# Optimization experiments

Hardware: AMD Instinct MI355X
Metric: run time of the kernel (lower is better)

Reference implementation:

```python
import jax, jax.numpy as jnp
import numpy as np

N = 100000
E = 800000
IN_CH = 128
HID = 32
HEADS = 8
OUT_CH = 40
NEG_SLOPE = 0.2


def setup_inputs() -> dict:
    key = jax.random.key(0)
    ks = jax.random.split(key, 10)
    x = jax.random.normal(ks[0], (N, IN_CH), dtype=jnp.float32)
    edge_index = jax.random.randint(ks[1], (2, E), 0, N, dtype=jnp.int64)
    # GATConv layer 1: in -> heads*hid, concat=True
    s1 = 1.0 / np.sqrt(IN_CH)
    W1 = jax.random.uniform(ks[2], (IN_CH, HEADS * HID), jnp.float32, -s1, s1)
    att_src1 = jax.random.uniform(ks[3], (1, HEADS, HID), jnp.float32, -s1, s1)
    att_dst1 = jax.random.uniform(ks[4], (1, HEADS, HID), jnp.float32, -s1, s1)
    b1 = jnp.zeros((HEADS * HID,), jnp.float32)
    # GATConv layer 2: heads*hid -> out, heads=1, concat=True
    s2 = 1.0 / np.sqrt(HEADS * HID)
    W2 = jax.random.uniform(ks[5], (HEADS * HID, OUT_CH), jnp.float32, -s2, s2)
    att_src2 = jax.random.uniform(ks[6], (1, 1, OUT_CH), jnp.float32, -s2, s2)
    att_dst2 = jax.random.uniform(ks[7], (1, 1, OUT_CH), jnp.float32, -s2, s2)
    b2 = jnp.zeros((OUT_CH,), jnp.float32)
    return {"x": x, "edge_index": edge_index,
            "W1": W1, "att_src1": att_src1, "att_dst1": att_dst1, "b1": b1,
            "W2": W2, "att_src2": att_src2, "att_dst2": att_dst2, "b2": b2}


def _gat_layer(x, src, dst, W, att_src, att_dst, bias, heads, out_ch):
    n = x.shape[0]
    xp = (x @ W).reshape(n, heads, out_ch)               # [N,H,C]
    a_src = jnp.sum(xp * att_src, axis=-1)               # [N,H]
    a_dst = jnp.sum(xp * att_dst, axis=-1)               # [N,H]
    logits = a_src[src] + a_dst[dst]                      # [Etot,H]
    logits = jnp.where(logits > 0, logits, NEG_SLOPE * logits)  # leaky_relu
    # segment softmax over destination node
    m = jax.ops.segment_max(logits, dst, num_segments=n)  # [N,H]
    p = jnp.exp(logits - m[dst])
    z = jax.ops.segment_sum(p, dst, num_segments=n)
    alpha = p / (z[dst] + 1e-16)                           # [Etot,H]
    out = jax.ops.segment_sum(xp[src] * alpha[:, :, None], dst, num_segments=n)
    return out.reshape(n, heads * out_ch) + bias


def reference(x, edge_index, W1, att_src1, att_dst1, b1, W2, att_src2, att_dst2, b2):
    n = x.shape[0]
    # add self loops (PyG GATConv default add_self_loops=True)
    loop = jnp.arange(n, dtype=edge_index.dtype)
    src = jnp.concatenate([edge_index[0], loop])
    dst = jnp.concatenate([edge_index[1], loop])
    # dropout p=0.2 is identity in eval mode
    h = _gat_layer(x, src, dst, W1, att_src1, att_dst1, b1, HEADS, HID)
    h = jax.nn.relu(h)
    out = _gat_layer(h, src, dst, W2, att_src2, att_dst2, b2, 1, OUT_CH)
    return jax.nn.log_softmax(out, axis=1)
```

## Files before the change

### kernel.cpp

```cpp
#include <hip/hip_runtime.h>
#include <math.h>

#define NN 100000
#define NE 800000
#define C1 256
#define OC 40
#define XPAD 64
#define NEG 0.2f
#define FCHUNK 4096
#define G1BLK 1563

typedef _Float16 h4 __attribute__((ext_vector_type(4)));
typedef _Float16 h8 __attribute__((ext_vector_type(8)));
typedef float f4v __attribute__((ext_vector_type(4)));
typedef float f2v __attribute__((ext_vector_type(2)));

static __device__ __forceinline__ float leaky(float v){ return v > 0.f ? v : NEG*v; }

static __device__ __forceinline__ h8 mk8(float4 a, float4 b){
  h8 r = {(_Float16)a.x,(_Float16)a.y,(_Float16)a.z,(_Float16)a.w,
          (_Float16)b.x,(_Float16)b.y,(_Float16)b.z,(_Float16)b.w};
  return r;
}

static __device__ __forceinline__ void gload_lds16(const float* g, float* l){
  __builtin_amdgcn_global_load_lds((const __attribute__((address_space(1))) void*)g,
                                   (__attribute__((address_space(3))) void*)l, 16, 0, 0);
}


__global__ __launch_bounds__(256) void k_wt(const float* __restrict__ W1, const float* __restrict__ W2,
                                            const float* __restrict__ aS1, const float* __restrict__ aD1,
                                            const float* __restrict__ aS2, const float* __restrict__ aD2,
                                            _Float16* __restrict__ W1t, _Float16* __restrict__ W2t,
                                            int* __restrict__ deg){
  int b = blockIdx.x;
  if (b < 128){
    int k = b, nb = threadIdx.x;
    W1t[(size_t)nb*128 + k] = (_Float16)W1[k*256 + nb];
  } else if (b < 176){
    int nb = b - 128;
    int e = threadIdx.x;
    int l = e >> 2, j = e & 3;
    int k = (l>>5)*128 + ((l>>4)&1)*64 + j*16 + (l&15);
    float v = (nb < OC) ? W2[(size_t)k*OC + nb] : 0.f;
    W2t[(size_t)nb*256 + e] = (_Float16)v;
  } else if (b < 178){
    int b2 = b - 176;
    int h  = threadIdx.x >> 5;
    int kb = (threadIdx.x & 31) * 4;
    const float* att = b2 ? aD1 : aS1;
    #pragma unroll
    for (int kk = 0; kk < 4; ++kk){
      int k = kb + kk;
      float s = 0.f;
      for (int c = 0; c < 32; ++c) s += W1[k*256 + h*32 + c] * att[h*32 + c];
      W1t[(size_t)(256 + b2*8 + h)*128 + k] = (_Float16)s;
    }
  } else if (b < 194){
    int j = b - 178;
    int e = threadIdx.x;
    int l = e >> 2, jj = e & 3;
    int k = (l>>5)*128 + ((l>>4)&1)*64 + jj*16 + (l&15);
    float v = 0.f;
    if (j == 0){ for (int c = 0; c < OC; ++c) v += W2[(size_t)k*OC + c] * aS2[c]; }
    else if (j == 1){ for (int c = 0; c < OC; ++c) v += W2[(size_t)k*OC + c] * aD2[c]; }
    W2t[(size_t)(48 + j)*256 + e] = (_Float16)v;
  } else {
    int i = (b - 194)*256 + threadIdx.x;
    if (i < NN) deg[i] = 1;
  }
}

__global__ __launch_bounds__(256) void k_gemm1(const float* __restrict__ x,
    const _Float16* __restrict__ W1t, unsigned* __restrict__ xp1w,
    float* __restrict__ asrc, float* __restrict__ adst,
    const int* __restrict__ ei, int* __restrict__ deg)
{
  __shared__ float xs[64*128];
  if (blockIdx.x >= G1BLK){
    int i = (blockIdx.x - G1BLK)*256 + threadIdx.x;
    if (i < NE) atomicAdd(&deg[ei[NE + i]], 1);
    return;
  }
  const int tid  = threadIdx.x;
  const int lane = tid & 63;
  const int w    = tid >> 6;
  const int wr = w >> 1, wc = w & 1;
  const int n = lane & 15, quad = lane >> 4;
  const int r0 = blockIdx.x * 64;

  if (r0 + 64 <= NN){
    #pragma unroll
    for (int it = 0; it < 8; ++it){
      int idx = it*256 + tid;
      int row = idx >> 5, c16 = idx & 31;
      const float* src = x + (size_t)(r0 + row)*128 + ((c16 ^ (row & 7)) << 2);
      gload_lds16(src, xs + ((size_t)(it*256 + w*64) << 2));
    }
  } else {
    #pragma unroll
    for (int it = 0; it < 8; ++it){
      int idx = it*256 + tid;
      int row = idx >> 5, c16 = idx & 31;
      int gr = r0 + row; gr = gr < NN ? gr : NN-1;
      ((float4*)xs)[idx] = *(const float4*)(x + (size_t)gr*128 + ((c16 ^ (row & 7)) << 2));
    }
  }

  h8 b0[9];
  #pragma unroll
  for (int ct = 0; ct < 8; ++ct)
    b0[ct] = *(const h8*)(W1t + (size_t)(wc*128 + ct*16 + n)*128 + quad*8);
  if (wc == 0) b0[8] = *(const h8*)(W1t + (size_t)(256 + n)*128 + quad*8);

  __syncthreads();

  f4v acc[2][8];
  #pragma unroll
  for (int rt = 0; rt < 2; ++rt)
    #pragma unroll
    for (int ct = 0; ct < 8; ++ct) acc[rt][ct] = (f4v){0.f,0.f,0.f,0.f};
  f4v accE0 = {0.f,0.f,0.f,0.f}, accE1 = {0.f,0.f,0.f,0.f};

  const int rowA = wr*32 + n;
  const int rowB = rowA + 16;
  const int s = n & 7;

  #pragma unroll
  for (int ks = 0; ks < 4; ++ks){
    const int base16 = ks*8 + quad*2;
    float4 fa0 = ((const float4*)xs)[rowA*32 + ((base16    ) ^ s)];
    float4 fa1 = ((const float4*)xs)[rowA*32 + ((base16 + 1) ^ s)];
    float4 fb0 = ((const float4*)xs)[rowB*32 + ((base16    ) ^ s)];
    float4 fb1 = ((const float4*)xs)[rowB*32 + ((base16 + 1) ^ s)];
    h8 a0 = mk8(fa0, fa1);
    h8 a1 = mk8(fb0, fb1);
    #pragma unroll
    for (int ct = 0; ct < 8; ++ct){
      h8 b = (ks == 0) ? b0[ct]
           : *(const h8*)(W1t + (size_t)(wc*128 + ct*16 + n)*128 + ks*32 + quad*8);
      acc[0][ct] = __builtin_amdgcn_mfma_f32_16x16x32_f16(a0, b, acc[0][ct], 0, 0, 0);
      acc[1][ct] = __builtin_amdgcn_mfma_f32_16x16x32_f16(a1, b, acc[1][ct], 0, 0, 0);
    }
    if (wc == 0){
      h8 b = (ks == 0) ? b0[8]
           : *(const h8*)(W1t + (size_t)(256 + n)*128 + ks*32 + quad*8);
      accE0 = __builtin_amdgcn_mfma_f32_16x16x32_f16(a0, b, accE0, 0, 0, 0);
      accE1 = __builtin_amdgcn_mfma_f32_16x16x32_f16(a1, b, accE1, 0, 0, 0);
    }
  }

  #pragma unroll
  for (int rt = 0; rt < 2; ++rt){
    #pragma unroll
    for (int reg = 0; reg < 4; ++reg){
      const int row = r0 + wr*32 + rt*16 + quad*4 + reg;
      if (row < NN){
        float v[8];
        #pragma unroll
        for (int ct = 0; ct < 8; ++ct) v[ct] = acc[rt][ct][reg];
        unsigned dwA = (unsigned)__builtin_amdgcn_cvt_pk_fp8_f32(v[0], v[1], 0, false);
        dwA = (unsigned)__builtin_amdgcn_cvt_pk_fp8_f32(v[2], v[3], (int)dwA, true);
        unsigned dwB = (unsigned)__builtin_amdgcn_cvt_pk_fp8_f32(v[4], v[5], 0, false);
        dwB = (unsigned)__builtin_amdgcn_cvt_pk_fp8_f32(v[6], v[7], (int)dwB, true);
        unsigned* xr = xp1w + (size_t)row*64 + wc*32 + n;
        xr[0]  = dwA;
        xr[16] = dwB;
        if (wc == 0){
          float vE = (rt == 0) ? accE0[reg] : accE1[reg];
          if (n < 8) asrc[row*8 + n] = vE;
          else       adst[row*8 + (n - 8)] = vE;
        }
      }
    }
  }
}

__global__ __launch_bounds__(256) void k_scan1(const int* __restrict__ deg, int* part, int* bsum){
  __shared__ int lds[256];
  const int t = threadIdx.x;
  const int base = blockIdx.x*1024;
  int v[4]; int s = 0;
  #pragma unroll
  for (int i = 0; i < 4; ++i){ int idx = base + t*4 + i; v[i] = (idx < NN) ? deg[idx] : 0; s += v[i]; }
  lds[t] = s; __syncthreads();
  for (int off = 1; off < 256; off <<= 1){
    int xx = (t >= off) ? lds[t-off] : 0;
    __syncthreads();
    lds[t] += xx;
    __syncthreads();
  }
  int excl = lds[t] - s;
  #pragma unroll
  for (int i = 0; i < 4; ++i){ int idx = base + t*4 + i; if (idx < NN) part[idx] = excl; excl += v[i]; }
  if (t == 255) bsum[blockIdx.x] = lds[255];
}
__global__ void k_scan2(const int* __restrict__ bsum, int* boff){
  const int l = threadIdx.x;
  int a = (l      < 98) ? bsum[l]      : 0;
  int b = (64 + l < 98) ? bsum[64 + l] : 0;
  int sa = a, sb = b;
  #pragma unroll
  for (int off = 1; off < 64; off <<= 1){
    int ta = __shfl_up(sa, off, 64);
    int tb = __shfl_up(sb, off, 64);
    if (l >= off){ sa += ta; sb += tb; }
  }
  const int totalA = __shfl(sa, 63, 64);
  if (l      < 98) boff[l]      = sa - a;
  if (64 + l < 98) boff[64 + l] = totalA + sb - b;
}
__global__ __launch_bounds__(256) void k_scan3(const int* __restrict__ part, const int* __restrict__ boff,
                                               int* rowptr, int* cursor){
  int i = blockIdx.x*256 + threadIdx.x;
  if (i < NN){ int v = part[i] + boff[i >> 10]; rowptr[i] = v; cursor[i] = v; }
  if (i == 0) rowptr[NN] = NN + NE;
}
__global__ __launch_bounds__(256) void k_fill(const int* __restrict__ ei, int* cursor, int* __restrict__ esrc){
  const int xcd = blockIdx.x & 7;
  const int base = (blockIdx.x >> 3) * FCHUNK;
  const int lo = xcd * (NN/8), hi = lo + (NN/8);
  const int end = (base + FCHUNK < NE + NN) ? (base + FCHUNK) : (NE + NN);
  for (int i = base + threadIdx.x; i < end; i += 256){
    int s, d;
    if (i < NE){ s = ei[i]; d = ei[NE + i]; } else { s = d = i - NE; }
    if (d >= lo && d < hi){
      int slot = atomicAdd(&cursor[d], 1);
      esrc[slot] = s;
    }
  }
}

template<int B>
static __device__ __forceinline__ void agg1_batch(
    const int j0, const int je, const int lane,
    const int* __restrict__ esrc, const float* __restrict__ asrc,
    const float adA, const float adB,
    const unsigned* __restrict__ xp1w,
    f2v& accLo, f2v& accHi, float& z0, float& z1)
{
  const int cnt = je - j0;
  const int slot = lane & 15;
  const int hA = (lane >> 4) << 1;
  int idx = j0 + slot; idx = idx < je ? idx : je - 1;
  const int sv = esrc[idx];
  float pv0 = 0.f, pv1 = 0.f;
  if (slot < cnt){
    f2v av = *(const f2v*)(asrc + (size_t)sv*8 + hA);
    pv0 = __expf(leaky(av.x + adA));
    pv1 = __expf(leaky(av.y + adB));
  }
  z0 += pv0; z1 += pv1;
  unsigned u[B];
  #pragma unroll
  for (int e = 0; e < B; ++e){
    int s = __builtin_amdgcn_readlane(sv, e);
    u[e] = xp1w[(size_t)s*64 + lane];
  }
  __builtin_amdgcn_sched_barrier(0);
  const int pb = lane & 48;
  #pragma unroll
  for (int e = 0; e < B; ++e){
    const float pA = __shfl(pv0, pb | e, 64);
    const float pB = __shfl(pv1, pb | e, 64);
    f2v lo = __builtin_amdgcn_cvt_pk_f32_fp8((int)u[e], false);
    f2v hi = __builtin_amdgcn_cvt_pk_f32_fp8((int)u[e], true);
    accLo += (f2v){pA, pA} * lo;
    accHi += (f2v){pB, pB} * hi;
  }
}

__global__ __launch_bounds__(256) void k_agg1(const unsigned* __restrict__ xp1w,
    const float* __restrict__ asrc, const float* __restrict__ adst,
    const float* __restrict__ b1, const int* __restrict__ rowptr,
    const int* __restrict__ esrc, _Float16* __restrict__ h1)
{
  const int lane = threadIdx.x & 63;
  int n = __builtin_amdgcn_readfirstlane(blockIdx.x*4 + (threadIdx.x >> 6));
  const int hA = (lane >> 4) << 1;
  const f2v ad = *(const f2v*)(adst + (size_t)n*8 + hA);
  const int jb = rowptr[n], je = rowptr[n+1];
  const int cbase = (lane>>5)*128 + ((lane>>4)&1)*64 + (lane&15);
  const float bp0 = b1[cbase], bp1 = b1[cbase+16], bp2 = b1[cbase+32], bp3 = b1[cbase+48];
  f2v accLo = {0.f,0.f}, accHi = {0.f,0.f};
  float z0 = 0.f, z1 = 0.f;

  int j0 = jb;
  while (j0 < je){
    if (je - j0 > 8){
      agg1_batch<16>(j0, je, lane, esrc, asrc, ad.x, ad.y, xp1w, accLo, accHi, z0, z1);
      j0 += 16;
    } else {
      agg1_batch<8>(j0, je, lane, esrc, asrc, ad.x, ad.y, xp1w, accLo, accHi, z0, z1);
      j0 += 8;
    }
  }
  #pragma unroll
  for (int off = 1; off <= 8; off <<= 1){
    z0 += __shfl_xor(z0, off, 64);
    z1 += __shfl_xor(z1, off, 64);
  }
  const float invA = 1.f/(z0 + 1e-16f), invB = 1.f/(z1 + 1e-16f);
  h4 o = {(_Float16)fmaxf(accLo.x*invA + bp0, 0.f),
          (_Float16)fmaxf(accLo.y*invA + bp1, 0.f),
          (_Float16)fmaxf(accHi.x*invB + bp2, 0.f),
          (_Float16)fmaxf(accHi.y*invB + bp3, 0.f)};
  ((h4*)h1)[(size_t)n*64 + lane] = o;
}

__global__ __launch_bounds__(256) void k_gemm2(const _Float16* __restrict__ h1,
    const _Float16* __restrict__ W2t, _Float16* __restrict__ xp2,
    float* __restrict__ asrc2, float* __restrict__ adst2)
{
  const int tid  = threadIdx.x;
  const int lane = tid & 63;
  const int w    = tid >> 6;
  const int n = lane & 15, quad = lane >> 4;
  const int r0 = blockIdx.x * 64 + w*16;

  f4v acc[4];
  #pragma unroll
  for (int ct = 0; ct < 4; ++ct) acc[ct] = (f4v){0.f,0.f,0.f,0.f};

  int rr = r0 + n; rr = rr < NN ? rr : NN-1;

  #pragma unroll
  for (int ks = 0; ks < 8; ++ks){
    h8 a = *(const h8*)(h1 + (size_t)rr*256 + ks*32 + quad*8);
    #pragma unroll
    for (int ct = 0; ct < 4; ++ct){
      h8 b = *(const h8*)(W2t + (size_t)(ct*16 + n)*256 + ks*32 + quad*8);
      acc[ct] = __builtin_amdgcn_mfma_f32_16x16x32_f16(a, b, acc[ct], 0, 0, 0);
    }
  }

  #pragma unroll
  for (int reg = 0; reg < 4; ++reg){
    const int row = r0 + quad*4 + reg;
    if (row < NN){
      float v0 = acc[0][reg], v1 = acc[1][reg], v2 = acc[2][reg], v3 = acc[3][reg];
      _Float16* xr = xp2 + (size_t)row*XPAD + n;
      xr[0]  = (_Float16)v0;
      xr[16] = (_Float16)v1;
      if (n < 8) xr[32] = (_Float16)v2;
      if (n == 0) asrc2[row] = v3;
      if (n == 1) adst2[row] = v3;
    }
  }
}

__global__ __launch_bounds__(256) void k_agg2(const _Float16* __restrict__ xp2,
    const float* __restrict__ asrc2, const float* __restrict__ adst2,
    const float* __restrict__ b2, const int* __restrict__ rowptr,
    const int* __restrict__ esrc, float* __restrict__ out)
{
  const int lane = threadIdx.x & 63;
  const int g = lane >> 4;
  const int t = lane & 15;
  int n = __builtin_amdgcn_readfirstlane(blockIdx.x*4 + (threadIdx.x >> 6));
  const float ad = adst2[n];
  const int jb = rowptr[n], je = rowptr[n+1];
  f4v acc = {0.f,0.f,0.f,0.f};
  float zacc = 0.f;

  for (int j0 = jb; j0 < je; j0 += 16){
    const int cnt = je - j0;
    int idx = j0 + t; idx = idx < je ? idx : je - 1;
    const int sv = esrc[idx];
    const float pv = (t < cnt) ? __expf(leaky(asrc2[sv] + ad)) : 0.f;
    zacc += pv;
    h4 u[4];
    #pragma unroll
    for (int e4 = 0; e4 < 4; ++e4){
      int svg = __shfl(sv, e4*4 + g, 64);
      u[e4] = *(const h4*)(xp2 + (size_t)svg*XPAD + t*4);
    }
    __builtin_amdgcn_sched_barrier(0);
    #pragma unroll
    for (int e4 = 0; e4 < 4; ++e4){
      const float p = __shfl(pv, e4*4 + g, 64);
      acc.x += p*(float)u[e4].x;
      acc.y += p*(float)u[e4].y;
      acc.z += p*(float)u[e4].z;
      acc.w += p*(float)u[e4].w;
    }
  }
  #pragma unroll
  for (int off = 1; off <= 8; off <<= 1) zacc += __shfl_xor(zacc, off, 64);
  #pragma unroll
  for (int off = 16; off <= 32; off <<= 1){
    acc.x += __shfl_xor(acc.x, off, 64);
    acc.y += __shfl_xor(acc.y, off, 64);
    acc.z += __shfl_xor(acc.z, off, 64);
    acc.w += __shfl_xor(acc.w, off, 64);
  }
  const float inv = 1.f/(zacc + 1e-16f);
  const bool act = t < 10;
  float4 bv = act ? *(const float4*)(b2 + 4*t) : make_float4(0.f,0.f,0.f,0.f);
  float v0 = acc.x*inv + bv.x, v1 = acc.y*inv + bv.y;
  float v2 = acc.z*inv + bv.z, v3 = acc.w*inv + bv.w;
  float m = act ? fmaxf(fmaxf(v0,v1), fmaxf(v2,v3)) : -INFINITY;
  #pragma unroll
  for (int off = 1; off <= 8; off <<= 1) m = fmaxf(m, __shfl_xor(m, off, 64));
  float es = act ? (__expf(v0-m)+__expf(v1-m)+__expf(v2-m)+__expf(v3-m)) : 0.f;
  #pragma unroll
  for (int off = 1; off <= 8; off <<= 1) es += __shfl_xor(es, off, 64);
  if (lane < 10){
    float lse = m + __logf(es);
    float4 o = make_float4(v0-lse, v1-lse, v2-lse, v3-lse);
    *(float4*)(out + (size_t)n*OC + 4*t) = o;
  }
}

extern "C" void kernel_launch(void* const* d_in, const int* in_sizes, int n_in,
                              void* d_out, int out_size, void* d_ws, size_t ws_size,
                              hipStream_t stream)
{
  const float* x   = (const float*)d_in[0];
  const int*   ei  = (const int*)  d_in[1];
  const float* W1  = (const float*)d_in[2];
  const float* aS1 = (const float*)d_in[3];
  const float* aD1 = (const float*)d_in[4];
  const float* b1  = (const float*)d_in[5];
  const float* W2  = (const float*)d_in[6];
  const float* aS2 = (const float*)d_in[7];
  const float* aD2 = (const float*)d_in[8];
  const float* b2  = (const float*)d_in[9];
  float* out = (float*)d_out;

  char* wsp = (char*)d_ws;
  size_t off = 0;
  auto alloc = [&](size_t bytes){ void* p = wsp + off; off += (bytes + 255) & ~(size_t)255; return p; };
  unsigned* xp1w = (unsigned*)alloc((size_t)NN*C1);
  _Float16* h1  = (_Float16*)alloc((size_t)NN*C1*2);
  float* as1  = (float*)alloc((size_t)NN*8*4);
  float* ad1  = (float*)alloc((size_t)NN*8*4);
  float* as2  = (float*)alloc((size_t)NN*4);
  float* ad2  = (float*)alloc((size_t)NN*4);
  int* deg    = (int*)alloc((size_t)NN*4);
  int* part   = (int*)alloc((size_t)NN*4);
  int* rowptr = (int*)alloc((size_t)(NN+1)*4);
  int* cursor = (int*)alloc((size_t)NN*4);
  int* bsum   = (int*)alloc(98*4);
  int* boff   = (int*)alloc(98*4);
  int* esrc   = (int*)alloc((size_t)(NN+NE)*4);
  _Float16* W1t = (_Float16*)alloc((size_t)272*128*2);
  _Float16* W2t = (_Float16*)alloc((size_t)64*256*2);
  _Float16* xp2 = (_Float16*)alloc((size_t)NN*XPAD*2);
  (void)ws_size; (void)in_sizes; (void)n_in; (void)out_size;

  const int fill_chunks = (NE + NN + FCHUNK - 1) / FCHUNK;
  const int deg_blocks  = (NE + 255) / 256;

  k_wt    <<<194 + (NN + 255)/256, 256, 0, stream>>>(W1, W2, aS1, aD1, aS2, aD2, W1t, W2t, deg);
  k_gemm1 <<<G1BLK + deg_blocks,   256, 0, stream>>>(x, W1t, xp1w, as1, ad1, ei, deg);
  k_scan1 <<<98,   256, 0, stream>>>(deg, part, bsum);
  k_scan2 <<<1,    64,  0, stream>>>(bsum, boff);
  k_scan3 <<<391,  256, 0, stream>>>(part, boff, rowptr, cursor);
  k_fill  <<<fill_chunks*8, 256, 0, stream>>>(ei, cursor, esrc);
  k_agg1  <<<25000,256, 0, stream>>>(xp1w, as1, ad1, b1, rowptr, esrc, h1);
  k_gemm2 <<<1563, 256, 0, stream>>>(h1, W2t, xp2, as2, ad2);
  k_agg2  <<<25000,256, 0, stream>>>(xp2, as2, ad2, b2, rowptr, esrc, out);
}
```

Measured before the change: 337.5 us.

## Restructure layer-1 GEMM to per-wave 16-row tiles loading x directly to registers

Replaces the shared-memory staged 64x128 x tile (loaded via global_load_lds with swizzle) with each wave loading its own 16 rows of x straight into registers. Each wave now computes all 256 output columns plus the attention column (17 MFMA tiles), so there is no LDS usage and no __syncthreads. This removes LDS traffic and the barrier and may raise occupancy, at the cost of each wave reading all of W1t (more global/L2 traffic for weights) and holding 17 accumulators in registers.

```diff
diff --git a/kernel.cpp b/kernel.cpp
--- a/kernel.cpp
+++ b/kernel.cpp
@@ -21,11 +21,6 @@
   h8 r = {(_Float16)a.x,(_Float16)a.y,(_Float16)a.z,(_Float16)a.w,
           (_Float16)b.x,(_Float16)b.y,(_Float16)b.z,(_Float16)b.w};
   return r;
-}
-
-static __device__ __forceinline__ void gload_lds16(const float* g, float* l){
-  __builtin_amdgcn_global_load_lds((const __attribute__((address_space(1))) void*)g,
-                                   (__attribute__((address_space(3))) void*)l, 16, 0, 0);
 }
 
 
@@ -77,7 +72,6 @@
     float* __restrict__ asrc, float* __restrict__ adst,
     const int* __restrict__ ei, int* __restrict__ deg)
 {
-  __shared__ float xs[64*128];
   if (blockIdx.x >= G1BLK){
     int i = (blockIdx.x - G1BLK)*256 + threadIdx.x;
     if (i < NE) atomicAdd(&deg[ei[NE + i]], 1);
@@ -86,93 +80,57 @@
   const int tid  = threadIdx.x;
   const int lane = tid & 63;
   const int w    = tid >> 6;
-  const int wr = w >> 1, wc = w & 1;
   const int n = lane & 15, quad = lane >> 4;
-  const int r0 = blockIdx.x * 64;
-
-  if (r0 + 64 <= NN){
+  const int r0 = blockIdx.x * 64 + w*16;
+
+  int ra = r0 + n; ra = ra < NN ? ra : NN-1;
+  const float* xr = x + (size_t)ra*128 + quad*8;
+
+  float4 fa[4][2];
+  #pragma unroll
+  for (int ks = 0; ks < 4; ++ks){
+    fa[ks][0] = *(const float4*)(xr + ks*32);
+    fa[ks][1] = *(const float4*)(xr + ks*32 + 4);
+  }
+
+  f4v acc[17];
+  #pragma unroll
+  for (int ct = 0; ct < 17; ++ct) acc[ct] = (f4v){0.f,0.f,0.f,0.f};
+
+  #pragma unroll
+  for (int ks = 0; ks < 4; ++ks){
+    h8 a = mk8(fa[ks][0], fa[ks][1]);
     #pragma unroll
-    for (int it = 0; it < 8; ++it){
-      int idx = it*256 + tid;
-      int row = idx >> 5, c16 = idx & 31;
-      const float* src = x + (size_t)(r0 + row)*128 + ((c16 ^ (row & 7)) << 2);
-      gload_lds16(src, xs + ((size_t)(it*256 + w*64) << 2));
-    }
-  } else {
-    #pragma unroll
-    for (int it = 0; it < 8; ++it){
-      int idx = it*256 + tid;
-      int row = idx >> 5, c16 = idx & 31;
-      int gr = r0 + row; gr = gr < NN ? gr : NN-1;
-      ((float4*)xs)[idx] = *(const float4*)(x + (size_t)gr*128 + ((c16 ^ (row & 7)) << 2));
-    }
-  }
-
-  h8 b0[9];
-  #pragma unroll
-  for (int ct = 0; ct < 8; ++ct)
-    b0[ct] = *(const h8*)(W1t + (size_t)(wc*128 + ct*16 + n)*128 + quad*8);
-  if (wc == 0) b0[8] = *(const h8*)(W1t + (size_t)(256 + n)*128 + quad*8);
-
-  __syncthreads();
-
-  f4v acc[2][8];
-  #pragma unroll
-  for (int rt = 0; rt < 2; ++rt)
-    #pragma unroll
-    for (int ct = 0; ct < 8; ++ct) acc[rt][ct] = (f4v){0.f,0.f,0.f,0.f};
-  f4v accE0 = {0.f,0.f,0.f,0.f}, accE1 = {0.f,0.f,0.f,0.f};
-
-  const int rowA = wr*32 + n;
-  const int rowB = rowA + 16;
-  const int s = n & 7;
-
-  #pragma unroll
-  for (int ks = 0; ks < 4; ++ks){
-    const int base16 = ks*8 + quad*2;
-    float4 fa0 = ((const float4*)xs)[rowA*32 + ((base16    ) ^ s)];
-    float4 fa1 = ((const float4*)xs)[rowA*32 + ((base16 + 1) ^ s)];
-    float4 fb0 = ((const float4*)xs)[rowB*32 + ((base16    ) ^ s)];
-    float4 fb1 = ((const float4*)xs)[rowB*32 + ((base16 + 1) ^ s)];
-    h8 a0 = mk8(fa0, fa1);
-    h8 a1 = mk8(fb0, fb1);
-    #pragma unroll
-    for (int ct = 0; ct < 8; ++ct){
-      h8 b = (ks == 0) ? b0[ct]
-           : *(const h8*)(W1t + (size_t)(wc*128 + ct*16 + n)*128 + ks*32 + quad*8);
-      acc[0][ct] = __builtin_amdgcn_mfma_f32_16x16x32_f16(a0, b, acc[0][ct], 0, 0, 0);
-      acc[1][ct] = __builtin_amdgcn_mfma_f32_16x16x32_f16(a1, b, acc[1][ct], 0, 0, 0);
-    }
-    if (wc == 0){
-      h8 b = (ks == 0) ? b0[8]
-           : *(const h8*)(W1t + (size_t)(256 + n)*128 + ks*32 + quad*8);
-      accE0 = __builtin_amdgcn_mfma_f32_16x16x32_f16(a0, b, accE0, 0, 0, 0);
-      accE1 = __builtin_amdgcn_mfma_f32_16x16x32_f16(a1, b, accE1, 0, 0, 0);
-    }
-  }
-
-  #pragma unroll
-  for (int rt = 0; rt < 2; ++rt){
-    #pragma unroll
-    for (int reg = 0; reg < 4; ++reg){
-      const int row = r0 + wr*32 + rt*16 + quad*4 + reg;
-      if (row < NN){
-        float v[8];
-        #pragma unroll
-        for (int ct = 0; ct < 8; ++ct) v[ct] = acc[rt][ct][reg];
-        unsigned dwA = (unsigned)__builtin_amdgcn_cvt_pk_fp8_f32(v[0], v[1], 0, false);
-        dwA = (unsigned)__builtin_amdgcn_cvt_pk_fp8_f32(v[2], v[3], (int)dwA, true);
-        unsigned dwB = (unsigned)__builtin_amdgcn_cvt_pk_fp8_f32(v[4], v[5], 0, false);
-        dwB = (unsigned)__builtin_amdgcn_cvt_pk_fp8_f32(v[6], v[7], (int)dwB, true);
-        unsigned* xr = xp1w + (size_t)row*64 + wc*32 + n;
-        xr[0]  = dwA;
-        xr[16] = dwB;
-        if (wc == 0){
-          float vE = (rt == 0) ? accE0[reg] : accE1[reg];
-          if (n < 8) asrc[row*8 + n] = vE;
-          else       adst[row*8 + (n - 8)] = vE;
-        }
-      }
+    for (int ct = 0; ct < 17; ++ct){
+      const int col = (ct < 16) ? (ct*16 + n) : (256 + n);
+      h8 b = *(const h8*)(W1t + (size_t)col*128 + ks*32 + quad*8);
+      acc[ct] = __builtin_amdgcn_mfma_f32_16x16x32_f16(a, b, acc[ct], 0, 0, 0);
+    }
+  }
+
+  #pragma unroll
+  for (int reg = 0; reg < 4; ++reg){
+    const int row = r0 + quad*4 + reg;
+    if (row < NN){
+      float v[16];
+      #pragma unroll
+      for (int ct = 0; ct < 16; ++ct) v[ct] = acc[ct][reg];
+      unsigned dw0 = (unsigned)__builtin_amdgcn_cvt_pk_fp8_f32(v[0], v[1], 0, false);
+      dw0 = (unsigned)__builtin_amdgcn_cvt_pk_fp8_f32(v[2], v[3], (int)dw0, true);
+      unsigned dw1 = (unsigned)__builtin_amdgcn_cvt_pk_fp8_f32(v[4], v[5], 0, false);
+      dw1 = (unsigned)__builtin_amdgcn_cvt_pk_fp8_f32(v[6], v[7], (int)dw1, true);
+      unsigned dw2 = (unsigned)__builtin_amdgcn_cvt_pk_fp8_f32(v[8], v[9], 0, false);
+      dw2 = (unsigned)__builtin_amdgcn_cvt_pk_fp8_f32(v[10], v[11], (int)dw2, true);
+      unsigned dw3 = (unsigned)__builtin_amdgcn_cvt_pk_fp8_f32(v[12], v[13], 0, false);
+      dw3 = (unsigned)__builtin_amdgcn_cvt_pk_fp8_f32(v[14], v[15], (int)dw3, true);
+      unsigned* xw = xp1w + (size_t)row*64;
+      xw[n]      = dw0;
+      xw[16 + n] = dw1;
+      xw[32 + n] = dw2;
+      xw[48 + n] = dw3;
+      float vE = acc[16][reg];
+      if (n < 8) asrc[row*8 + n] = vE;
+      else       adst[row*8 + (n - 8)] = vE;
     }
   }
 }
```

After: 355.6 us. 5.4% more time.
